# Kernel optimization log

Measured on AMD Instinct MI355X. Metric: run time of the kernel, lower is better.

## Reference

```python
import jax, jax.numpy as jnp
import numpy as np

N_VAR = 100000
N_CON = 100000
N_EDGE = 2000000
C = 32  # all channel widths


def _linear(x, W, b):
    return x @ W.T + b


def setup_inputs() -> dict:
    key = jax.random.key(0)
    ks = jax.random.split(key, 16)
    s = 1.0 / np.sqrt(C)
    se = 1.0 / np.sqrt(3 * C)
    inp = {
        "var_f": jax.random.normal(ks[0], (N_VAR, C), jnp.float32),
        "con_f": jax.random.normal(ks[1], (N_CON, C), jnp.float32),
        "combined_edge_f": jax.random.normal(ks[2], (N_EDGE, C), jnp.float32),
        "edge_index_var_con": jax.random.randint(ks[3], (2, N_EDGE), 0, N_VAR, jnp.int32),
        # var_compress_mlp
        "Wv1": jax.random.uniform(ks[4], (C, C), jnp.float32, -s, s),
        "bv1": jnp.zeros((C,), jnp.float32),
        "Wv2": jax.random.uniform(ks[5], (C, C), jnp.float32, -s, s),
        "bv2": jnp.zeros((C,), jnp.float32),
        # con_compress_mlp
        "Wc1": jax.random.uniform(ks[6], (C, C), jnp.float32, -s, s),
        "bc1": jnp.zeros((C,), jnp.float32),
        "Wc2": jax.random.uniform(ks[7], (C, C), jnp.float32, -s, s),
        "bc2": jnp.zeros((C,), jnp.float32),
        # edge_mlp (input width = 3*C)
        "We1": jax.random.uniform(ks[8], (C, 3 * C), jnp.float32, -se, se),
        "be1": jnp.zeros((C,), jnp.float32),
        "We2": jax.random.uniform(ks[9], (C, C), jnp.float32, -s, s),
        "be2": jnp.zeros((C,), jnp.float32),
    }
    return inp


def reference(var_f, con_f, combined_edge_f, edge_index_var_con,
              Wv1, bv1, Wv2, bv2, Wc1, bc1, Wc2, bc2, We1, be1, We2, be2):
    # compress node features with 2-layer ReLU MLPs (done on nodes, not edges)
    v = jax.nn.relu(_linear(jax.nn.relu(_linear(var_f, Wv1, bv1)), Wv2, bv2))
    c = jax.nn.relu(_linear(jax.nn.relu(_linear(con_f, Wc1, bc1)), Wc2, bc2))
    # gather per-edge and concat: [E, 3C]
    out = jnp.concatenate(
        [combined_edge_f, v[edge_index_var_con[0]], c[edge_index_var_con[1]]], axis=1)
    # edge MLP: Linear -> ReLU -> Linear (no final ReLU)
    return _linear(jax.nn.relu(_linear(out, We1, be1)), We2, be2)
```

## Files before the change

kernel.cpp:

```cpp
#include <hip/hip_runtime.h>

typedef float  f32x2  __attribute__((ext_vector_type(2)));
typedef float  f32x4  __attribute__((ext_vector_type(4)));
typedef float  f32x16 __attribute__((ext_vector_type(16)));
typedef short  s16x4  __attribute__((ext_vector_type(4)));
typedef short  s16x8  __attribute__((ext_vector_type(8)));
typedef unsigned int u32x2 __attribute__((ext_vector_type(2)));

__device__ __forceinline__ unsigned f2bf(float f) {
    unsigned u = __builtin_bit_cast(unsigned, f);
    u += 0x7FFFu + ((u >> 16) & 1u);
    return u >> 16;
}
__device__ __forceinline__ s16x4 pack4(float a, float b, float c, float d) {
    u32x2 u;
    u[0] = f2bf(a) | (f2bf(b) << 16);
    u[1] = f2bf(c) | (f2bf(d) << 16);
    return __builtin_bit_cast(s16x4, u);
}
__device__ __forceinline__ s16x4 lo4(s16x8 v) { return __builtin_shufflevector(v, v, 0, 1, 2, 3); }
__device__ __forceinline__ s16x4 hi4(s16x8 v) { return __builtin_shufflevector(v, v, 4, 5, 6, 7); }

__global__ __launch_bounds__(256) void node_kernel(
    const float* __restrict__ X,
    const float* __restrict__ W1, const float* __restrict__ b1,
    const float* __restrict__ W2, const float* __restrict__ b2,
    const float* __restrict__ Wm, int wm_stride, const float* __restrict__ bm,
    unsigned short* __restrict__ outp, int N)
{
    const int lane = threadIdx.x & 63;
    const int g = lane >> 5, m = lane & 31;
    const int ntile = (N + 31) >> 5;
    const int tile = (blockIdx.x * blockDim.x + threadIdx.x) >> 6;
    if (tile >= ntile) return;

    s16x4 a1[4], a2[4], am[4];
#pragma unroll
    for (int q = 0; q < 4; ++q) {
        const float* p1 = W1 + m * 32 + 8 * q + 4 * g;
        a1[q] = pack4(p1[0], p1[1], p1[2], p1[3]);
        const float* p2 = W2 + m * 32 + 8 * q + 4 * g;
        a2[q] = pack4(p2[0], p2[1], p2[2], p2[3]);
        const float* pm = Wm + m * wm_stride + 8 * q + 4 * g;
        am[q] = pack4(pm[0], pm[1], pm[2], pm[3]);
    }
    f32x16 f1, f2, f3;
#pragma unroll
    for (int r = 0; r < 16; ++r) {
        int ch = (r & 3) + 8 * (r >> 2) + 4 * g;
        f1[r] = b1[ch];
        f2[r] = b2[ch];
        f3[r] = bm ? bm[ch] : 0.f;
    }

    const int node0 = tile * 32 + m;
    const int node = node0 < N ? node0 : N - 1;

    s16x4 bX[4];
#pragma unroll
    for (int q = 0; q < 4; ++q) {
        f32x4 v = *reinterpret_cast<const f32x4*>(X + (size_t)node * 32 + 8 * q + 4 * g);
        bX[q] = pack4(v[0], v[1], v[2], v[3]);
    }
    f32x16 acc = f1;
#pragma unroll
    for (int q = 0; q < 4; ++q) acc = __builtin_amdgcn_mfma_f32_32x32x8bf16_1k(a1[q], bX[q], acc, 0, 0, 0);
    s16x4 bH[4];
#pragma unroll
    for (int q = 0; q < 4; ++q)
        bH[q] = pack4(fmaxf(acc[4*q+0], 0.f), fmaxf(acc[4*q+1], 0.f),
                      fmaxf(acc[4*q+2], 0.f), fmaxf(acc[4*q+3], 0.f));
    acc = f2;
#pragma unroll
    for (int q = 0; q < 4; ++q) acc = __builtin_amdgcn_mfma_f32_32x32x8bf16_1k(a2[q], bH[q], acc, 0, 0, 0);
#pragma unroll
    for (int q = 0; q < 4; ++q)
        bH[q] = pack4(fmaxf(acc[4*q+0], 0.f), fmaxf(acc[4*q+1], 0.f),
                      fmaxf(acc[4*q+2], 0.f), fmaxf(acc[4*q+3], 0.f));
    acc = f3;
#pragma unroll
    for (int q = 0; q < 4; ++q) acc = __builtin_amdgcn_mfma_f32_32x32x8bf16_1k(am[q], bH[q], acc, 0, 0, 0);

    if (node0 < N) {
#pragma unroll
        for (int q = 0; q < 4; ++q) {
            s16x4 o = pack4(acc[4*q+0], acc[4*q+1], acc[4*q+2], acc[4*q+3]);
            *reinterpret_cast<s16x4*>(outp + (size_t)node0 * 32 + 8 * q + 4 * g) = o;
        }
    }
}

__device__ __forceinline__ void stage_tile(const float* __restrict__ Ef, float* buf,
                                           int tile, int wv, int a, int b) {
    const float* src = Ef + (size_t)tile * 4096 + (size_t)(wv * 32 + a) * 32 + ((b ^ a) << 2);
    float* dst = buf + wv * 1024;
#pragma unroll
    for (int j = 0; j < 4; ++j) {
        __builtin_amdgcn_global_load_lds(
            (const __attribute__((address_space(1))) unsigned int*)(src + j * 256),
            (__attribute__((address_space(3))) unsigned int*)(dst + j * 256),
            16, 0, 0);
    }
}

__global__ __launch_bounds__(256) void edge_kernel(
    const float* __restrict__ Ef, const int* __restrict__ idx,
    const unsigned short* __restrict__ pv, const unsigned short* __restrict__ pc,
    const float* __restrict__ We1, const float* __restrict__ We2,
    const float* __restrict__ be2,
    float* __restrict__ out, int nE)
{
    __shared__ float lds[2 * 4096 + 128 * 34];
    float* ldso = lds + 8192;

    const int lane = threadIdx.x & 63;
    const int wv = threadIdx.x >> 6;
    const int g = lane >> 5, n = lane & 31;
    const int a = lane >> 3, b = lane & 7;

    s16x4 aW1[4], aI[4], aW2[4];
#pragma unroll
    for (int q = 0; q < 4; ++q) {
        const float* p = We1 + n * 96 + 16 * g + 4 * q;
        aW1[q] = pack4(p[0], p[1], p[2], p[3]);
        s16x4 r;
#pragma unroll
        for (int j = 0; j < 4; ++j) r[j] = (short)((16 * g + 4 * q + j == n) ? 0x3F80 : 0);
        aI[q] = r;
        const float* p2 = We2 + n * 32 + 8 * q + 4 * g;
        aW2[q] = pack4(p2[0], p2[1], p2[2], p2[3]);
    }
    f32x16 bias2;
#pragma unroll
    for (int r = 0; r < 16; ++r) bias2[r] = be2[(r & 3) + 8 * (r >> 2) + 4 * g];

    const int tiles = nE >> 7;
    int t = blockIdx.x;
    if (t >= tiles) return;
    int cur = 0;

    stage_tile(Ef, lds, t, wv, a, b);
    int e = t * 128 + wv * 32 + n;
    int i0 = idx[e], i1 = idx[nE + e];

    while (true) {
        const int tn = t + gridDim.x;
        __syncthreads();
        if (tn < tiles) stage_tile(Ef, lds + (cur ^ 1) * 4096, tn, wv, a, b);

        const unsigned short* pvr = pv + (size_t)i0 * 32 + 16 * g;
        const unsigned short* pcr = pc + (size_t)i1 * 32 + 16 * g;
        s16x8 v0 = *reinterpret_cast<const s16x8*>(pvr);
        s16x8 v1 = *reinterpret_cast<const s16x8*>(pvr + 8);
        s16x8 c0 = *reinterpret_cast<const s16x8*>(pcr);
        s16x8 c1 = *reinterpret_cast<const s16x8*>(pcr + 8);

        int i0n = 0, i1n = 0;
        if (tn < tiles) {
            int en = tn * 128 + wv * 32 + n;
            i0n = idx[en];
            i1n = idx[nE + en];
        }

        const float* efb = lds + cur * 4096 + (size_t)(wv * 32 + n) * 32;
        f32x16 acc = {};
        s16x4 bE[4];
#pragma unroll
        for (int q = 0; q < 4; ++q) {
            f32x4 v = *reinterpret_cast<const f32x4*>(efb + (((4 * g + q) ^ (n & 7)) << 2));
            bE[q] = pack4(v[0], v[1], v[2], v[3]);
        }
#pragma unroll
        for (int q = 0; q < 4; ++q) acc = __builtin_amdgcn_mfma_f32_32x32x8bf16_1k(aW1[q], bE[q], acc, 0, 0, 0);
        acc = __builtin_amdgcn_mfma_f32_32x32x8bf16_1k(aI[0], lo4(v0), acc, 0, 0, 0);
        acc = __builtin_amdgcn_mfma_f32_32x32x8bf16_1k(aI[1], hi4(v0), acc, 0, 0, 0);
        acc = __builtin_amdgcn_mfma_f32_32x32x8bf16_1k(aI[2], lo4(v1), acc, 0, 0, 0);
        acc = __builtin_amdgcn_mfma_f32_32x32x8bf16_1k(aI[3], hi4(v1), acc, 0, 0, 0);
        acc = __builtin_amdgcn_mfma_f32_32x32x8bf16_1k(aI[0], lo4(c0), acc, 0, 0, 0);
        acc = __builtin_amdgcn_mfma_f32_32x32x8bf16_1k(aI[1], hi4(c0), acc, 0, 0, 0);
        acc = __builtin_amdgcn_mfma_f32_32x32x8bf16_1k(aI[2], lo4(c1), acc, 0, 0, 0);
        acc = __builtin_amdgcn_mfma_f32_32x32x8bf16_1k(aI[3], hi4(c1), acc, 0, 0, 0);

        s16x4 bH[4];
#pragma unroll
        for (int q = 0; q < 4; ++q)
            bH[q] = pack4(fmaxf(acc[4*q+0], 0.f), fmaxf(acc[4*q+1], 0.f),
                          fmaxf(acc[4*q+2], 0.f), fmaxf(acc[4*q+3], 0.f));
        f32x16 acc2 = bias2;
#pragma unroll
        for (int q = 0; q < 4; ++q) acc2 = __builtin_amdgcn_mfma_f32_32x32x8bf16_1k(aW2[q], bH[q], acc2, 0, 0, 0);

        {
            float* orow = ldso + (size_t)(wv * 32 + n) * 34;
#pragma unroll
            for (int q = 0; q < 4; ++q) {
                f32x2 lo; lo[0] = acc2[4*q+0]; lo[1] = acc2[4*q+1];
                f32x2 hi; hi[0] = acc2[4*q+2]; hi[1] = acc2[4*q+3];
                *reinterpret_cast<f32x2*>(orow + 8 * q + 4 * g)     = lo;
                *reinterpret_cast<f32x2*>(orow + 8 * q + 4 * g + 2) = hi;
            }
        }
        __syncthreads();

        {
            const int T = threadIdx.x;
            const size_t obase = (size_t)t * 4096;
#pragma unroll
            for (int p = 0; p < 4; ++p) {
                int w = p * 1024 + T * 4;
                int row = w >> 5, col = w & 31;
                const float* s = ldso + (size_t)row * 34 + col;
                f32x2 lo = *reinterpret_cast<const f32x2*>(s);
                f32x2 hi = *reinterpret_cast<const f32x2*>(s + 2);
                f32x4 v; v[0] = lo[0]; v[1] = lo[1]; v[2] = hi[0]; v[3] = hi[1];
                __builtin_nontemporal_store(v, reinterpret_cast<f32x4*>(out + obase + w));
            }
        }

        if (tn >= tiles) break;
        t = tn; cur ^= 1; i0 = i0n; i1 = i1n;
    }
}

extern "C" void kernel_launch(void* const* d_in, const int* in_sizes, int n_in,
                              void* d_out, int out_size, void* d_ws, size_t ws_size,
                              hipStream_t stream) {
    const float* var_f = (const float*)d_in[0];
    const float* con_f = (const float*)d_in[1];
    const float* Ef    = (const float*)d_in[2];
    const int*   idx   = (const int*)d_in[3];
    const float* Wv1 = (const float*)d_in[4];
    const float* bv1 = (const float*)d_in[5];
    const float* Wv2 = (const float*)d_in[6];
    const float* bv2 = (const float*)d_in[7];
    const float* Wc1 = (const float*)d_in[8];
    const float* bc1 = (const float*)d_in[9];
    const float* Wc2 = (const float*)d_in[10];
    const float* bc2 = (const float*)d_in[11];
    const float* We1 = (const float*)d_in[12];
    const float* be1 = (const float*)d_in[13];
    const float* We2 = (const float*)d_in[14];
    const float* be2 = (const float*)d_in[15];
    float* out = (float*)d_out;

    const int nV = in_sizes[0] / 32;
    const int nC = in_sizes[1] / 32;
    const int nE = in_sizes[2] / 32;

    unsigned short* pv = (unsigned short*)d_ws;
    unsigned short* pc = pv + (size_t)nV * 32;

    {
        int ntileV = (nV + 31) >> 5;
        int blocksV = (ntileV * 64 + 255) / 256;
        node_kernel<<<blocksV, 256, 0, stream>>>(var_f, Wv1, bv1, Wv2, bv2,
                                                 We1 + 32, 96, be1, pv, nV);
        int ntileC = (nC + 31) >> 5;
        int blocksC = (ntileC * 64 + 255) / 256;
        node_kernel<<<blocksC, 256, 0, stream>>>(con_f, Wc1, bc1, Wc2, bc2,
                                                 We1 + 64, 96, nullptr, pc, nC);
    }
    edge_kernel<<<1024, 256, 0, stream>>>(Ef, idx, pv, pc, We1, We2, be2, out, nE);
}
```

Baseline: 171.8 us.

## Stream edge features via register prefetch per wave, merge node kernels into one launch

The edge kernel drops block-wide LDS double buffering and __syncthreads. Each wave now owns a 32-edge tile, prefetches the next tile's indices and edge features into registers with nontemporal loads, and stages its output through a private LDS slice. The two node-MLP launches are merged into one kernel that picks the var or con path from the block index. The second-layer bias is folded into an extra rank-one MFMA. This removes barrier stalls and one launch, at the cost of more registers per thread (launch_bounds minimum blocks set to 4) and less contiguous edge-feature loads per wave.

Result: slower. 195.9 us (+14.0%).

```diff
diff --git a/kernel.cpp b/kernel.cpp
--- a/kernel.cpp
+++ b/kernel.cpp
@@ -18,20 +18,20 @@
     u[1] = f2bf(c) | (f2bf(d) << 16);
     return __builtin_bit_cast(s16x4, u);
 }
+__device__ __forceinline__ s16x4 pack4v(f32x4 v) { return pack4(v[0], v[1], v[2], v[3]); }
 __device__ __forceinline__ s16x4 lo4(s16x8 v) { return __builtin_shufflevector(v, v, 0, 1, 2, 3); }
 __device__ __forceinline__ s16x4 hi4(s16x8 v) { return __builtin_shufflevector(v, v, 4, 5, 6, 7); }
 
-__global__ __launch_bounds__(256) void node_kernel(
+__device__ __forceinline__ void node_body(
     const float* __restrict__ X,
     const float* __restrict__ W1, const float* __restrict__ b1,
     const float* __restrict__ W2, const float* __restrict__ b2,
-    const float* __restrict__ Wm, int wm_stride, const float* __restrict__ bm,
-    unsigned short* __restrict__ outp, int N)
+    const float* __restrict__ Wm, const float* __restrict__ bm,
+    unsigned short* __restrict__ outp, int N, int tile)
 {
     const int lane = threadIdx.x & 63;
     const int g = lane >> 5, m = lane & 31;
     const int ntile = (N + 31) >> 5;
-    const int tile = (blockIdx.x * blockDim.x + threadIdx.x) >> 6;
     if (tile >= ntile) return;
 
     s16x4 a1[4], a2[4], am[4];
@@ -41,7 +41,7 @@
         a1[q] = pack4(p1[0], p1[1], p1[2], p1[3]);
         const float* p2 = W2 + m * 32 + 8 * q + 4 * g;
         a2[q] = pack4(p2[0], p2[1], p2[2], p2[3]);
-        const float* pm = Wm + m * wm_stride + 8 * q + 4 * g;
+        const float* pm = Wm + m * 96 + 8 * q + 4 * g;
         am[q] = pack4(pm[0], pm[1], pm[2], pm[3]);
     }
     f32x16 f1, f2, f3;
@@ -60,7 +60,7 @@
 #pragma unroll
     for (int q = 0; q < 4; ++q) {
         f32x4 v = *reinterpret_cast<const f32x4*>(X + (size_t)node * 32 + 8 * q + 4 * g);
-        bX[q] = pack4(v[0], v[1], v[2], v[3]);
+        bX[q] = pack4v(v);
     }
     f32x16 acc = f1;
 #pragma unroll
@@ -90,33 +90,37 @@
     }
 }
 
-__device__ __forceinline__ void stage_tile(const float* __restrict__ Ef, float* buf,
-                                           int tile, int wv, int a, int b) {
-    const float* src = Ef + (size_t)tile * 4096 + (size_t)(wv * 32 + a) * 32 + ((b ^ a) << 2);
-    float* dst = buf + wv * 1024;
-#pragma unroll
-    for (int j = 0; j < 4; ++j) {
-        __builtin_amdgcn_global_load_lds(
-            (const __attribute__((address_space(1))) unsigned int*)(src + j * 256),
-            (__attribute__((address_space(3))) unsigned int*)(dst + j * 256),
-            16, 0, 0);
-    }
-}
-
-__global__ __launch_bounds__(256) void edge_kernel(
+__global__ __launch_bounds__(256) void nodes_kernel(
+    const float* __restrict__ var_f, const float* __restrict__ con_f,
+    const float* __restrict__ Wv1, const float* __restrict__ bv1,
+    const float* __restrict__ Wv2, const float* __restrict__ bv2,
+    const float* __restrict__ Wc1, const float* __restrict__ bc1,
+    const float* __restrict__ Wc2, const float* __restrict__ bc2,
+    const float* __restrict__ We1, const float* __restrict__ be1,
+    unsigned short* __restrict__ pv, unsigned short* __restrict__ pc,
+    int nV, int nC, int blocksV)
+{
+    const int wv = threadIdx.x >> 6;
+    if ((int)blockIdx.x < blocksV) {
+        node_body(var_f, Wv1, bv1, Wv2, bv2, We1 + 32, be1, pv, nV, blockIdx.x * 4 + wv);
+    } else {
+        node_body(con_f, Wc1, bc1, Wc2, bc2, We1 + 64, nullptr, pc, nC,
+                  (blockIdx.x - blocksV) * 4 + wv);
+    }
+}
+
+__global__ __launch_bounds__(256, 4) void edge_kernel(
     const float* __restrict__ Ef, const int* __restrict__ idx,
     const unsigned short* __restrict__ pv, const unsigned short* __restrict__ pc,
     const float* __restrict__ We1, const float* __restrict__ We2,
     const float* __restrict__ be2,
     float* __restrict__ out, int nE)
 {
-    __shared__ float lds[2 * 4096 + 128 * 34];
-    float* ldso = lds + 8192;
-
+    __shared__ float ldso[4 * 1088];
     const int lane = threadIdx.x & 63;
     const int wv = threadIdx.x >> 6;
     const int g = lane >> 5, n = lane & 31;
-    const int a = lane >> 3, b = lane & 7;
+    float* ldsw = ldso + wv * 1088;
 
     s16x4 aW1[4], aI[4], aW2[4];
 #pragma unroll
@@ -130,68 +134,77 @@
         const float* p2 = We2 + n * 32 + 8 * q + 4 * g;
         aW2[q] = pack4(p2[0], p2[1], p2[2], p2[3]);
     }
-    f32x16 bias2;
-#pragma unroll
-    for (int r = 0; r < 16; ++r) bias2[r] = be2[(r & 3) + 8 * (r >> 2) + 4 * g];
-
-    const int tiles = nE >> 7;
-    int t = blockIdx.x;
-    if (t >= tiles) return;
-    int cur = 0;
-
-    stage_tile(Ef, lds, t, wv, a, b);
-    int e = t * 128 + wv * 32 + n;
-    int i0 = idx[e], i1 = idx[nE + e];
+    s16x4 aB2 = {}, bOne = {};
+    if (g == 0) {
+        aB2[0] = (short)f2bf(be2[n]);
+        bOne[0] = (short)0x3F80;
+    }
+
+    const int ntile = nE >> 5;
+    const int nw = (gridDim.x * blockDim.x) >> 6;
+    int t = (blockIdx.x * blockDim.x + threadIdx.x) >> 6;
+    if (t >= ntile) return;
+
+    int e = t * 32 + n;
+    int i0c = __builtin_nontemporal_load(idx + e);
+    int i1c = __builtin_nontemporal_load(idx + nE + e);
+    const float* efp = Ef + (size_t)e * 32 + 16 * g;
+    f32x4 ef0 = __builtin_nontemporal_load(reinterpret_cast<const f32x4*>(efp + 0));
+    f32x4 ef1 = __builtin_nontemporal_load(reinterpret_cast<const f32x4*>(efp + 4));
+    f32x4 ef2 = __builtin_nontemporal_load(reinterpret_cast<const f32x4*>(efp + 8));
+    f32x4 ef3 = __builtin_nontemporal_load(reinterpret_cast<const f32x4*>(efp + 12));
 
     while (true) {
-        const int tn = t + gridDim.x;
-        __syncthreads();
-        if (tn < tiles) stage_tile(Ef, lds + (cur ^ 1) * 4096, tn, wv, a, b);
-
-        const unsigned short* pvr = pv + (size_t)i0 * 32 + 16 * g;
-        const unsigned short* pcr = pc + (size_t)i1 * 32 + 16 * g;
-        s16x8 v0 = *reinterpret_cast<const s16x8*>(pvr);
-        s16x8 v1 = *reinterpret_cast<const s16x8*>(pvr + 8);
-        s16x8 c0 = *reinterpret_cast<const s16x8*>(pcr);
-        s16x8 c1 = *reinterpret_cast<const s16x8*>(pcr + 8);
-
-        int i0n = 0, i1n = 0;
-        if (tn < tiles) {
-            int en = tn * 128 + wv * 32 + n;
-            i0n = idx[en];
-            i1n = idx[nE + en];
+        const int tn = t + nw;
+        const int tc = tn < ntile ? tn : t;
+
+        const unsigned short* pvr = pv + (size_t)i0c * 32 + 16 * g;
+        const unsigned short* pcr = pc + (size_t)i1c * 32 + 16 * g;
+        s16x8 gv0 = *reinterpret_cast<const s16x8*>(pvr);
+        s16x8 gv1 = *reinterpret_cast<const s16x8*>(pvr + 8);
+        s16x8 gc0 = *reinterpret_cast<const s16x8*>(pcr);
+        s16x8 gc1 = *reinterpret_cast<const s16x8*>(pcr + 8);
+
+        const int en = tc * 32 + n;
+        int i0n = __builtin_nontemporal_load(idx + en);
+        int i1n = __builtin_nontemporal_load(idx + nE + en);
+        const float* efpn = Ef + (size_t)en * 32 + 16 * g;
+        f32x4 efn0 = __builtin_nontemporal_load(reinterpret_cast<const f32x4*>(efpn + 0));
+        f32x4 efn1 = __builtin_nontemporal_load(reinterpret_cast<const f32x4*>(efpn + 4));
+        f32x4 efn2 = __builtin_nontemporal_load(reinterpret_cast<const f32x4*>(efpn + 8));
+        f32x4 efn3 = __builtin_nontemporal_load(reinterpret_cast<const f32x4*>(efpn + 12));
+
+        f32x16 acc = {};
+        {
+            s16x4 bE0 = pack4v(ef0), bE1 = pack4v(ef1), bE2 = pack4v(ef2), bE3 = pack4v(ef3);
+            acc = __builtin_amdgcn_mfma_f32_32x32x8bf16_1k(aW1[0], bE0, acc, 0, 0, 0);
+            acc = __builtin_amdgcn_mfma_f32_32x32x8bf16_1k(aW1[1], bE1, acc, 0, 0, 0);
+            acc = __builtin_amdgcn_mfma_f32_32x32x8bf16_1k(aW1[2], bE2, acc, 0, 0, 0);
+            acc = __builtin_amdgcn_mfma_f32_32x32x8bf16_1k(aW1[3], bE3, acc, 0, 0, 0);
         }
-
-        const float* efb = lds + cur * 4096 + (size_t)(wv * 32 + n) * 32;
-        f32x16 acc = {};
-        s16x4 bE[4];
-#pragma unroll
-        for (int q = 0; q < 4; ++q) {
-            f32x4 v = *reinterpret_cast<const f32x4*>(efb + (((4 * g + q) ^ (n & 7)) << 2));
-            bE[q] = pack4(v[0], v[1], v[2], v[3]);
-        }
-#pragma unroll
-        for (int q = 0; q < 4; ++q) acc = __builtin_amdgcn_mfma_f32_32x32x8bf16_1k(aW1[q], bE[q], acc, 0, 0, 0);
-        acc = __builtin_amdgcn_mfma_f32_32x32x8bf16_1k(aI[0], lo4(v0), acc, 0, 0, 0);
-        acc = __builtin_amdgcn_mfma_f32_32x32x8bf16_1k(aI[1], hi4(v0), acc, 0, 0, 0);
-        acc = __builtin_amdgcn_mfma_f32_32x32x8bf16_1k(aI[2], lo4(v1), acc, 0, 0, 0);
-        acc = __builtin_amdgcn_mfma_f32_32x32x8bf16_1k(aI[3], hi4(v1), acc, 0, 0, 0);
-        acc = __builtin_amdgcn_mfma_f32_32x32x8bf16_1k(aI[0], lo4(c0), acc, 0, 0, 0);
-        acc = __builtin_amdgcn_mfma_f32_32x32x8bf16_1k(aI[1], hi4(c0), acc, 0, 0, 0);
-        acc = __builtin_amdgcn_mfma_f32_32x32x8bf16_1k(aI[2], lo4(c1), acc, 0, 0, 0);
-        acc = __builtin_amdgcn_mfma_f32_32x32x8bf16_1k(aI[3], hi4(c1), acc, 0, 0, 0);
+        acc = __builtin_amdgcn_mfma_f32_32x32x8bf16_1k(aI[0], lo4(gv0), acc, 0, 0, 0);
+        acc = __builtin_amdgcn_mfma_f32_32x32x8bf16_1k(aI[1], hi4(gv0), acc, 0, 0, 0);
+        acc = __builtin_amdgcn_mfma_f32_32x32x8bf16_1k(aI[2], lo4(gv1), acc, 0, 0, 0);
+        acc = __builtin_amdgcn_mfma_f32_32x32x8bf16_1k(aI[3], hi4(gv1), acc, 0, 0, 0);
+        acc = __builtin_amdgcn_mfma_f32_32x32x8bf16_1k(aI[0], lo4(gc0), acc, 0, 0, 0);
+        acc = __builtin_amdgcn_mfma_f32_32x32x8bf16_1k(aI[1], hi4(gc0), acc, 0, 0, 0);
+        acc = __builtin_amdgcn_mfma_f32_32x32x8bf16_1k(aI[2], lo4(gc1), acc, 0, 0, 0);
+        acc = __builtin_amdgcn_mfma_f32_32x32x8bf16_1k(aI[3], hi4(gc1), acc, 0, 0, 0);
 
         s16x4 bH[4];
 #pragma unroll
         for (int q = 0; q < 4; ++q)
             bH[q] = pack4(fmaxf(acc[4*q+0], 0.f), fmaxf(acc[4*q+1], 0.f),
                           fmaxf(acc[4*q+2], 0.f), fmaxf(acc[4*q+3], 0.f));
-        f32x16 acc2 = bias2;
-#pragma unroll
-        for (int q = 0; q < 4; ++q) acc2 = __builtin_amdgcn_mfma_f32_32x32x8bf16_1k(aW2[q], bH[q], acc2, 0, 0, 0);
+
+        f32x16 acc2 = {};
+        acc2 = __builtin_amdgcn_mfma_f32_32x32x8bf16_1k(aB2, bOne, acc2, 0, 0, 0);
+#pragma unroll
+        for (int q = 0; q < 4; ++q)
+            acc2 = __builtin_amdgcn_mfma_f32_32x32x8bf16_1k(aW2[q], bH[q], acc2, 0, 0, 0);
 
         {
-            float* orow = ldso + (size_t)(wv * 32 + n) * 34;
+            float* orow = ldsw + n * 34;
 #pragma unroll
             for (int q = 0; q < 4; ++q) {
                 f32x2 lo; lo[0] = acc2[4*q+0]; lo[1] = acc2[4*q+1];
@@ -199,26 +212,23 @@
                 *reinterpret_cast<f32x2*>(orow + 8 * q + 4 * g)     = lo;
                 *reinterpret_cast<f32x2*>(orow + 8 * q + 4 * g + 2) = hi;
             }
-        }
-        __syncthreads();
-
-        {
-            const int T = threadIdx.x;
-            const size_t obase = (size_t)t * 4096;
+            float* obase = out + (size_t)t * 1024;
 #pragma unroll
             for (int p = 0; p < 4; ++p) {
-                int w = p * 1024 + T * 4;
-                int row = w >> 5, col = w & 31;
-                const float* s = ldso + (size_t)row * 34 + col;
+                int li = p * 256 + lane * 4;
+                int row = li >> 5, col = li & 31;
+                const float* s = ldsw + row * 34 + col;
                 f32x2 lo = *reinterpret_cast<const f32x2*>(s);
                 f32x2 hi = *reinterpret_cast<const f32x2*>(s + 2);
                 f32x4 v; v[0] = lo[0]; v[1] = lo[1]; v[2] = hi[0]; v[3] = hi[1];
-                __builtin_nontemporal_store(v, reinterpret_cast<f32x4*>(out + obase + w));
+                __builtin_nontemporal_store(v, reinterpret_cast<f32x4*>(obase + li));
             }
         }
 
-        if (tn >= tiles) break;
-        t = tn; cur ^= 1; i0 = i0n; i1 = i1n;
+        if (tn >= ntile) break;
+        t = tn;
+        i0c = i0n; i1c = i1n;
+        ef0 = efn0; ef1 = efn1; ef2 = efn2; ef3 = efn3;
     }
 }
 
@@ -250,15 +260,11 @@
     unsigned short* pv = (unsigned short*)d_ws;
     unsigned short* pc = pv + (size_t)nV * 32;
 
-    {
-        int ntileV = (nV + 31) >> 5;
-        int blocksV = (ntileV * 64 + 255) / 256;
-        node_kernel<<<blocksV, 256, 0, stream>>>(var_f, Wv1, bv1, Wv2, bv2,
-                                                 We1 + 32, 96, be1, pv, nV);
-        int ntileC = (nC + 31) >> 5;
-        int blocksC = (ntileC * 64 + 255) / 256;
-        node_kernel<<<blocksC, 256, 0, stream>>>(con_f, Wc1, bc1, Wc2, bc2,
-                                                 We1 + 64, 96, nullptr, pc, nC);
-    }
+    const int blocksV = ((((nV + 31) >> 5) + 3) / 4);
+    const int blocksC = ((((nC + 31) >> 5) + 3) / 4);
+    nodes_kernel<<<blocksV + blocksC, 256, 0, stream>>>(
+        var_f, con_f, Wv1, bv1, Wv2, bv2, Wc1, bc1, Wc2, bc2,
+        We1, be1, pv, pc, nV, nC, blocksV);
+
     edge_kernel<<<1024, 256, 0, stream>>>(Ef, idx, pv, pc, We1, We2, be2, out, nE);
 }
```
